# Performance work log

Hardware: AMD Instinct MI355X
Metric: run time of the kernel (lower is better)

The kernel has to match this reference:

```python
import jax, jax.numpy as jnp
from jax import lax
import numpy as np

T = 100  # number of binarization thresholds, as in nn.Module (linspace(0,1,100))
THRESHOLDS = jnp.linspace(0.0, 1.0, T)


def _count_components(binimg):
    """4-connected component count per image via iterative min-label propagation.
    binimg: [N,H,W] float in {0,1}. Returns [N] int32 component counts.
    Equivalent math to the source's recursive DFS flood fill, vectorized."""
    N, H, W = binimg.shape
    fg = binimg > 0
    BIG = H * W  # sentinel label for background
    idx = jnp.arange(H * W, dtype=jnp.int32).reshape(H, W)
    lab0 = jnp.where(fg, idx[None], jnp.int32(BIG))

    def prop(lab):
        p = jnp.pad(lab, ((0, 0), (1, 1), (1, 1)), constant_values=BIG)
        nmin = jnp.minimum(jnp.minimum(p[:, :-2, 1:-1], p[:, 2:, 1:-1]),
                           jnp.minimum(p[:, 1:-1, :-2], p[:, 1:-1, 2:]))
        return jnp.where(fg, jnp.minimum(lab, nmin), jnp.int32(BIG))

    def cond(c):
        return ~c[1]

    def body(c):
        lab = c[0]
        new = prop(prop(prop(lab)))  # 3 propagation steps per convergence check
        return (new, jnp.all(new == lab))

    lab, _ = lax.while_loop(cond, body, (lab0, jnp.array(False)))
    # each component keeps exactly one pixel whose label equals its own index
    return jnp.sum(fg & (lab == idx[None]), axis=(1, 2)).astype(jnp.int32)


def _betti(prob):
    """prob: [R,H,W] -> [T,R,2] (b0, b1) per threshold per region.
    b1 = b0 - euler, euler = #pixels - #4-neighbor edges (as in source)."""
    R, H, W = prob.shape
    binz = (prob[None] > THRESHOLDS[:, None, None, None]).astype(jnp.float32)  # [T,R,H,W]
    flat = binz.reshape(T * R, H, W)
    b0 = lax.stop_gradient(_count_components(flat)).astype(jnp.float32).reshape(T, R)
    pix = flat.sum((1, 2))
    edges = (flat[:, :-1] * flat[:, 1:]).sum((1, 2)) + (flat[:, :, :-1] * flat[:, :, 1:]).sum((1, 2))
    euler = (pix - edges).reshape(T, R)
    b1 = b0 - euler
    return jnp.stack([b0, b1], axis=-1)  # [T,R,2]


def setup_inputs() -> dict:
    key = jax.random.key(0)
    k1, k2 = jax.random.split(key)
    three_class_prob = jax.random.uniform(k1, (4, 3, 128, 128), dtype=jnp.float32)
    selected_regions = jnp.arange(4, dtype=jnp.int64)
    gt_barcodes = jax.random.uniform(k2, (4, 6, T - 1, 2), dtype=jnp.float32)
    return {"three_class_prob": three_class_prob,
            "selected_regions": selected_regions,
            "gt_barcodes": gt_barcodes}


def reference(three_class_prob, selected_regions, gt_barcodes):
    sel = three_class_prob[selected_regions]  # [R,3,H,W]
    inside = _betti(sel[:, 0])     # channel 0
    boundary = _betti(sel[:, 1])   # channel 1
    union = inside                 # source uses channel 0:1 again -> same values
    codes = jnp.concatenate([inside, boundary, union], axis=-1)  # [T,R,6]
    # barcode extraction: birth at increases of the betti curve, death at decreases
    d = codes[1:] - codes[:-1]                 # [T-1,R,6]
    th = THRESHOLDS[:-1, None, None]
    birth = jnp.where(d > 0, th, 0.0)
    death = jnp.where(d < 0, th, 0.0)
    barcodes = jnp.stack([birth, death], axis=-1).transpose(1, 2, 0, 3)  # [R,6,T-1,2]
    # fixed-shape matching: pair barcodes sorted by birth time (Hungarian surrogate)
    ord_b = jnp.argsort(barcodes[..., 0], axis=-1)
    ord_g = jnp.argsort(gt_barcodes[..., 0], axis=-1)
    bs = jnp.take_along_axis(barcodes, ord_b[..., None], axis=-2)
    gs = jnp.take_along_axis(gt_barcodes, ord_g[..., None], axis=-2)
    matched_diff = jnp.sum(jnp.abs(bs - gs), axis=-1)                  # [R,6,T-1]
    unmatched_len = jnp.sum(barcodes[..., 1] - barcodes[..., 0], axis=-1)  # [R,6]
    return jnp.mean(matched_diff) + jnp.mean(unmatched_len)
```

## Files before the change

### kernel.cpp

```cpp
#include <hip/hip_runtime.h>

typedef unsigned long long u64;

__device__ __forceinline__ int find_root(int* L, int a){
    int p = L[a];
    while(p != a){
        int gp = L[p];
        if(gp != p) L[a] = gp;
        a = p; p = gp;
    }
    return a;
}

__device__ __forceinline__ int unite(int* L, int a, int b){
    while(true){
        a = find_root(L, a);
        b = find_root(L, b);
        if(a == b) return 0;
        int hi = (a > b) ? a : b;
        int lo = (a > b) ? b : a;
        int old = atomicCAS(&L[hi], hi, lo);
        if(old == hi) return 1;
        a = old; b = lo;
    }
}

__global__ __launch_bounds__(256) void ccl_kernel(const float* __restrict__ prob,
                                                  const int*   __restrict__ sel,
                                                  float*       __restrict__ betti,
                                                  float*       __restrict__ out){
    __shared__ u64 M[256];
    __shared__ u64 S[256];
    __shared__ int Pr[257];
    __shared__ int L[6400];
    __shared__ int red[12];
    const int tid = threadIdx.x, bid = blockIdx.x;
    if(bid == 0 && tid == 0) atomicExch(out, 0.0f);
    const int ch = bid / 400, t = (bid % 400) >> 2, r = bid & 3;
    const float th = (float)t / 99.0f;
    const float* img = prob + (size_t)(sel[r] * 3 + ch) * 16384;

    const int w = tid;
    {
        const float4* imgv = (const float4*)img;
        u64 mw = 0ULL;
        #pragma unroll
        for(int k = 0; k < 16; k++){
            const float4 v = imgv[w * 16 + k];
            const unsigned nib = (unsigned)(v.x > th)
                               | ((unsigned)(v.y > th) << 1)
                               | ((unsigned)(v.z > th) << 2)
                               | ((unsigned)(v.w > th) << 3);
            mw |= (u64)nib << (4 * k);
        }
        M[w] = mw;
    }
    __syncthreads();

    const int lane = tid & 63, wave = tid >> 6;
    const int row = w >> 1, half = w & 1;
    const u64 m = M[w];
    const u64 lcar = half ? (M[w - 1] >> 63) : 0ULL;
    const u64 s = m & ~((m << 1) | lcar);
    S[w] = s;
    int pix   = __popcll(m);
    int edges = __popcll(m & ((m << 1) | lcar));
    const u64 va = (row > 0) ? M[w - 2] : 0ULL;
    edges += __popcll(m & va);
    const int runs = __popcll(s);
    u64 csm = 0ULL;
    if(row > 0){
        const u64 c = m & va;
        const u64 ccar = half ? ((M[w - 1] & M[w - 3]) >> 63) : 0ULL;
        csm = c & ~((c << 1) | ccar);
    }

    int incl = runs;
    for(int off = 1; off < 64; off <<= 1){
        int n = __shfl_up(incl, off, 64);
        if(lane >= off) incl += n;
    }
    if(lane == 63) red[wave] = incl;
    __syncthreads();
    int woff = 0;
    for(int k = 0; k < wave; k++) woff += red[k];
    const int excl = woff + incl - runs;
    Pr[w] = excl;
    if(w == 255) Pr[256] = excl + runs;
    const u64 sa = (row > 0) ? S[w - 2] : 0ULL;
    __syncthreads();
    const int R = Pr[256];
    const int Pa = (row > 0) ? Pr[w - 2] : 0;

    {
        int4* L4 = (int4*)L;
        const int n4 = (R + 3) >> 2;
        for(int i = tid; i < n4; i += 256){ int b = i * 4; L4[i] = make_int4(b, b+1, b+2, b+3); }
    }
    __syncthreads();

    int merges = 0;
    {
        u64 cs = csm;
        while(cs){
            const int x = __ffsll(cs) - 1;
            cs &= cs - 1;
            const u64 lm = (2ULL << x) - 1;
            const int nb = excl + __popcll(s  & lm) - 1;
            const int na = Pa   + __popcll(sa & lm) - 1;
            merges += unite(L, na, nb);
        }
    }

    int v0 = pix, v1 = edges, v2 = merges;
    for(int off = 32; off; off >>= 1){
        v0 += __shfl_down(v0, off, 64);
        v1 += __shfl_down(v1, off, 64);
        v2 += __shfl_down(v2, off, 64);
    }
    __syncthreads();
    if(lane == 0){ red[wave*3] = v0; red[wave*3+1] = v1; red[wave*3+2] = v2; }
    __syncthreads();
    if(tid == 0){
        int P = 0, E = 0, MG = 0;
        for(int k = 0; k < 4; k++){ P += red[k*3]; E += red[k*3+1]; MG += red[k*3+2]; }
        const float b0f = (float)(R - MG);
        const float b1f = b0f - ((float)P - (float)E);
        const size_t o = (((size_t)ch * 100 + t) * 4 + r) * 2;
        betti[o] = b0f; betti[o + 1] = b1f;
    }
}

__global__ __launch_bounds__(128) void rows_kernel(const float* __restrict__ betti,
                                                   const float* __restrict__ gt,
                                                   float*       __restrict__ out){
    __shared__ float codes[100];
    __shared__ float birth[99], bs0[99], bs1[99], gs0[99], gs1[99];
    __shared__ float gsh[198];
    __shared__ float red[4];
    const int row = blockIdx.x;
    const int r = row / 6, j = row % 6;
    const int chmap[6] = {0, 0, 1, 1, 0, 0};
    const int ch = chmap[j], comp = j & 1;
    const int tid = threadIdx.x;

    if(tid < 100) codes[tid] = betti[(((size_t)ch * 100 + tid) * 4 + r) * 2 + comp];
    const float* g = gt + (size_t)row * 99 * 2;
    for(int i = tid; i < 198; i += 128) gsh[i] = g[i];
    __syncthreads();

    float b = 0.f, d = 0.f;
    if(tid < 99){
        const float dv = codes[tid + 1] - codes[tid];
        const float thv = (float)tid / 99.0f;
        b = (dv > 0.f) ? thv : 0.f;
        d = (dv < 0.f) ? thv : 0.f;
        birth[tid] = b;
    }
    __syncthreads();

    if(tid < 99){
        int zb = 0, tz = 0;
        for(int k = 0; k < 99; k++){
            const int z = (birth[k] == 0.f) ? 1 : 0;
            tz += z;
            if(k < tid) zb += z;
        }
        const int pos = (b == 0.f) ? zb : (tz + tid - zb);
        bs0[pos] = b; bs1[pos] = d;

        const float gb = gsh[tid * 2];
        int rank = 0;
        for(int k = 0; k < 99; k++){
            const float o = gsh[k * 2];
            rank += (o < gb || (o == gb && k < tid)) ? 1 : 0;
        }
        gs0[rank] = gb; gs1[rank] = gsh[tid * 2 + 1];
    }
    __syncthreads();

    float mm = 0.f, u = 0.f;
    if(tid < 99){
        mm = fabsf(bs0[tid] - gs0[tid]) + fabsf(bs1[tid] - gs1[tid]);
        u = d - b;
    }
    for(int off = 32; off; off >>= 1){
        mm += __shfl_down(mm, off, 64);
        u  += __shfl_down(u,  off, 64);
    }
    if((tid & 63) == 0){ red[(tid >> 6)*2] = mm; red[(tid >> 6)*2 + 1] = u; }
    __syncthreads();
    if(tid == 0)
        atomicAdd(out, (red[0] + red[2]) / 2376.0f + (red[1] + red[3]) / 24.0f);
}

extern "C" void kernel_launch(void* const* d_in, const int* in_sizes, int n_in,
                              void* d_out, int out_size, void* d_ws, size_t ws_size,
                              hipStream_t stream){
    const float* prob = (const float*)d_in[0];
    const int*   sel  = (const int*)d_in[1];
    const float* gt   = (const float*)d_in[2];
    float* betti = (float*)d_ws;

    ccl_kernel <<<800, 256, 0, stream>>>(prob, sel, betti, (float*)d_out);
    rows_kernel<<<24, 128, 0, stream>>>(betti, gt, (float*)d_out);
}
```

Measured before the change: 92.82 us.

## Compact vertical merge edges into per-wave shared lists before union-find

Each thread used to walk its own vertical run-overlap bits and call union-find serially, so lanes with many overlaps held back their whole wave. The change packs each wave's edge count into the existing prefix scan, writes every merge pair into a per-wave shared buffer (capacity 512), and then spreads the unite calls evenly across the 64 lanes. Pairs beyond the capacity fall back to the old inline path. This adds shared memory, which can lower occupancy, plus an extra barrier.

New measurement: 97.01 us. 4.5% more time.

```diff
diff --git a/kernel.cpp b/kernel.cpp
--- a/kernel.cpp
+++ b/kernel.cpp
@@ -1,6 +1,8 @@
 #include <hip/hip_runtime.h>
 
 typedef unsigned long long u64;
+
+#define ECAP 512
 
 __device__ __forceinline__ int find_root(int* L, int a){
     int p = L[a];
@@ -33,6 +35,7 @@
     __shared__ u64 S[256];
     __shared__ int Pr[257];
     __shared__ int L[6400];
+    __shared__ unsigned E[4*ECAP];
     __shared__ int red[12];
     const int tid = threadIdx.x, bid = blockIdx.x;
     if(bid == 0 && tid == 0) atomicExch(out, 0.0f);
@@ -74,17 +77,20 @@
         const u64 ccar = half ? ((M[w - 1] & M[w - 3]) >> 63) : 0ULL;
         csm = c & ~((c << 1) | ccar);
     }
-
-    int incl = runs;
+    const int cw = __popcll(csm);
+
+    int incl = runs | (cw << 16);
     for(int off = 1; off < 64; off <<= 1){
         int n = __shfl_up(incl, off, 64);
         if(lane >= off) incl += n;
     }
-    if(lane == 63) red[wave] = incl;
+    if(lane == 63) red[wave] = incl & 0xFFFF;
+    const int ewt = (__shfl(incl, 63, 64)) >> 16;
     __syncthreads();
     int woff = 0;
     for(int k = 0; k < wave; k++) woff += red[k];
-    const int excl = woff + incl - runs;
+    const int excl  = woff + (incl & 0xFFFF) - runs;
+    const int ebase = (incl >> 16) - cw;
     Pr[w] = excl;
     if(w == 255) Pr[256] = excl + runs;
     const u64 sa = (row > 0) ? S[w - 2] : 0ULL;
@@ -102,13 +108,25 @@
     int merges = 0;
     {
         u64 cs = csm;
+        int bi = ebase;
         while(cs){
             const int x = __ffsll(cs) - 1;
             cs &= cs - 1;
             const u64 lm = (2ULL << x) - 1;
             const int nb = excl + __popcll(s  & lm) - 1;
             const int na = Pa   + __popcll(sa & lm) - 1;
-            merges += unite(L, na, nb);
+            if(bi < ECAP) E[wave * ECAP + bi] = ((unsigned)na << 13) | (unsigned)nb;
+            else merges += unite(L, na, nb);
+            bi++;
+        }
+    }
+    __syncthreads();
+
+    {
+        const int ew = ewt < ECAP ? ewt : ECAP;
+        for(int j = lane; j < ew; j += 64){
+            const unsigned e = E[wave * ECAP + j];
+            merges += unite(L, (int)(e >> 13), (int)(e & 8191u));
         }
     }
 
@@ -122,10 +140,10 @@
     if(lane == 0){ red[wave*3] = v0; red[wave*3+1] = v1; red[wave*3+2] = v2; }
     __syncthreads();
     if(tid == 0){
-        int P = 0, E = 0, MG = 0;
-        for(int k = 0; k < 4; k++){ P += red[k*3]; E += red[k*3+1]; MG += red[k*3+2]; }
+        int P = 0, Eh = 0, MG = 0;
+        for(int k = 0; k < 4; k++){ P += red[k*3]; Eh += red[k*3+1]; MG += red[k*3+2]; }
         const float b0f = (float)(R - MG);
-        const float b1f = b0f - ((float)P - (float)E);
+        const float b1f = b0f - ((float)P - (float)Eh);
         const size_t o = (((size_t)ch * 100 + t) * 4 + r) * 2;
         betti[o] = b0f; betti[o + 1] = b1f;
     }
```

## Split CCL into half-image blocks with a separate seam-merge kernel

Applied to the files above, without the earlier changes.

Each 128x128 binarized image is now labeled by two 128-thread blocks, one per half. The boundary-row root labels, masks and per-half statistics go to workspace, and a new merge kernel unites components across the seam to compute b0 and b1. This doubles block count and shrinks shared memory per block to raise occupancy and parallelism. It costs an extra kernel launch, global round trips for the labels, and serial bit-skipping loops in the merge.

New measurement: 97.28 us. 1.05x slower.

```diff
diff --git a/kernel.cpp b/kernel.cpp
--- a/kernel.cpp
+++ b/kernel.cpp
@@ -25,24 +25,27 @@
     }
 }
 
-__global__ __launch_bounds__(256) void ccl_kernel(const float* __restrict__ prob,
-                                                  const int*   __restrict__ sel,
-                                                  float*       __restrict__ betti,
-                                                  float*       __restrict__ out){
-    __shared__ u64 M[256];
-    __shared__ u64 S[256];
-    __shared__ int Pr[257];
-    __shared__ int L[6400];
-    __shared__ int red[12];
+__global__ __launch_bounds__(128) void ccl_half(const float* __restrict__ prob,
+                                                const int*   __restrict__ sel,
+                                                int*   __restrict__ labs,
+                                                u64*   __restrict__ bmask,
+                                                int*   __restrict__ stats,
+                                                float* __restrict__ out){
+    __shared__ u64 M[128];
+    __shared__ u64 S[128];
+    __shared__ int Pr[129];
+    __shared__ int L[4096];
+    __shared__ int red[8];
     const int tid = threadIdx.x, bid = blockIdx.x;
     if(bid == 0 && tid == 0) atomicExch(out, 0.0f);
-    const int ch = bid / 400, t = (bid % 400) >> 2, r = bid & 3;
+    const int ib = bid >> 1, h = bid & 1;
+    const int ch = ib / 400, t = (ib % 400) >> 2, r = ib & 3;
     const float th = (float)t / 99.0f;
     const float* img = prob + (size_t)(sel[r] * 3 + ch) * 16384;
+    const float4* imgv = (const float4*)img + h * 2048;
 
     const int w = tid;
     {
-        const float4* imgv = (const float4*)img;
         u64 mw = 0ULL;
         #pragma unroll
         for(int k = 0; k < 16; k++){
@@ -58,18 +61,18 @@
     __syncthreads();
 
     const int lane = tid & 63, wave = tid >> 6;
-    const int row = w >> 1, half = w & 1;
+    const int lrow = w >> 1, half = w & 1;
     const u64 m = M[w];
     const u64 lcar = half ? (M[w - 1] >> 63) : 0ULL;
     const u64 s = m & ~((m << 1) | lcar);
     S[w] = s;
     int pix   = __popcll(m);
     int edges = __popcll(m & ((m << 1) | lcar));
-    const u64 va = (row > 0) ? M[w - 2] : 0ULL;
+    const u64 va = (lrow > 0) ? M[w - 2] : 0ULL;
     edges += __popcll(m & va);
     const int runs = __popcll(s);
     u64 csm = 0ULL;
-    if(row > 0){
+    if(lrow > 0){
         const u64 c = m & va;
         const u64 ccar = half ? ((M[w - 1] & M[w - 3]) >> 63) : 0ULL;
         csm = c & ~((c << 1) | ccar);
@@ -82,20 +85,19 @@
     }
     if(lane == 63) red[wave] = incl;
     __syncthreads();
-    int woff = 0;
-    for(int k = 0; k < wave; k++) woff += red[k];
+    const int woff = wave ? red[0] : 0;
     const int excl = woff + incl - runs;
     Pr[w] = excl;
-    if(w == 255) Pr[256] = excl + runs;
-    const u64 sa = (row > 0) ? S[w - 2] : 0ULL;
-    __syncthreads();
-    const int R = Pr[256];
-    const int Pa = (row > 0) ? Pr[w - 2] : 0;
+    if(w == 127) Pr[128] = excl + runs;
+    const u64 sa = (lrow > 0) ? S[w - 2] : 0ULL;
+    __syncthreads();
+    const int R = Pr[128];
+    const int Pa = (lrow > 0) ? Pr[w - 2] : 0;
 
     {
         int4* L4 = (int4*)L;
         const int n4 = (R + 3) >> 2;
-        for(int i = tid; i < n4; i += 256){ int b = i * 4; L4[i] = make_int4(b, b+1, b+2, b+3); }
+        for(int i = tid; i < n4; i += 128){ int b = i * 4; L4[i] = make_int4(b, b+1, b+2, b+3); }
     }
     __syncthreads();
 
@@ -111,6 +113,18 @@
             merges += unite(L, na, nb);
         }
     }
+    __syncthreads();
+
+    {
+        const int lo    = h ? 0 : Pr[126];
+        const int hiEnd = h ? Pr[2] : R;
+        for(int i = lo + tid; i < hiEnd; i += 128)
+            labs[(size_t)bid * 64 + (i - lo)] = find_root(L, i);
+        if(tid < 2){
+            const int bw = h ? tid : (126 + tid);
+            bmask[(size_t)bid * 2 + tid] = M[bw];
+        }
+    }
 
     int v0 = pix, v1 = edges, v2 = merges;
     for(int off = 32; off; off >>= 1){
@@ -122,10 +136,61 @@
     if(lane == 0){ red[wave*3] = v0; red[wave*3+1] = v1; red[wave*3+2] = v2; }
     __syncthreads();
     if(tid == 0){
-        int P = 0, E = 0, MG = 0;
-        for(int k = 0; k < 4; k++){ P += red[k*3]; E += red[k*3+1]; MG += red[k*3+2]; }
-        const float b0f = (float)(R - MG);
-        const float b1f = b0f - ((float)P - (float)E);
+        stats[(size_t)bid*3 + 0] = red[0] + red[3];
+        stats[(size_t)bid*3 + 1] = red[1] + red[4];
+        stats[(size_t)bid*3 + 2] = R - (red[2] + red[5]);
+    }
+}
+
+__global__ __launch_bounds__(64) void merge_kernel(const int* __restrict__ labs,
+                                                   const u64* __restrict__ bmask,
+                                                   const int* __restrict__ stats,
+                                                   float*     __restrict__ betti){
+    __shared__ int A[8192];
+    __shared__ int TL[64], BL[64];
+    const int ib = blockIdx.x, tid = threadIdx.x;
+    const int tb = ib * 2, bb = ib * 2 + 1;
+    const u64 t0 = bmask[(size_t)tb*2], t1 = bmask[(size_t)tb*2+1];
+    const u64 b0m = bmask[(size_t)bb*2], b1m = bmask[(size_t)bb*2+1];
+    const u64 st0 = t0 & ~(t0 << 1);
+    const u64 st1 = t1 & ~((t1 << 1) | (t0 >> 63));
+    const u64 sb0 = b0m & ~(b0m << 1);
+    const u64 sb1 = b1m & ~((b1m << 1) | (b0m >> 63));
+    const int nT = __popcll(st0) + __popcll(st1);
+    const int nB = __popcll(sb0) + __popcll(sb1);
+    if(tid < nT) TL[tid] = labs[(size_t)tb*64 + tid];
+    if(tid < nB) BL[tid] = labs[(size_t)bb*64 + tid];
+    __syncthreads();
+    if(tid < nT){ const int l = TL[tid];        A[l] = l; }
+    if(tid < nB){ const int l = BL[tid] + 4096; A[l] = l; }
+    __syncthreads();
+
+    const u64 c0 = t0 & b0m, c1 = t1 & b1m;
+    const u64 cs0 = c0 & ~(c0 << 1);
+    const u64 cs1 = c1 & ~((c1 << 1) | (c0 >> 63));
+    const int n0 = __popcll(cs0), nC = n0 + __popcll(cs1);
+    const int seamE = __popcll(c0) + __popcll(c1);
+
+    int merges = 0;
+    for(int j = tid; j < nC; j += 64){
+        u64 cs; int k, wv;
+        if(j < n0){ cs = cs0; wv = 0; k = j; } else { cs = cs1; wv = 1; k = j - n0; }
+        for(int q = 0; q < k; q++) cs &= cs - 1;
+        const int x = __ffsll(cs) - 1;
+        const u64 lm = (2ULL << x) - 1;
+        int it, ibx;
+        if(wv == 0){ it = __popcll(st0 & lm) - 1;                 ibx = __popcll(sb0 & lm) - 1; }
+        else       { it = __popcll(st0) + __popcll(st1 & lm) - 1; ibx = __popcll(sb0) + __popcll(sb1 & lm) - 1; }
+        merges += unite(A, TL[it], BL[ibx] + 4096);
+    }
+    for(int off = 32; off; off >>= 1) merges += __shfl_down(merges, off, 64);
+    if(tid == 0){
+        const int pix   = stats[(size_t)tb*3]   + stats[(size_t)bb*3];
+        const int edges = stats[(size_t)tb*3+1] + stats[(size_t)bb*3+1] + seamE;
+        const int b0    = stats[(size_t)tb*3+2] + stats[(size_t)bb*3+2] - merges;
+        const int ch = ib / 400, t = (ib % 400) >> 2, r = ib & 3;
+        const float b0f = (float)b0;
+        const float b1f = b0f - ((float)pix - (float)edges);
         const size_t o = (((size_t)ch * 100 + t) * 4 + r) * 2;
         betti[o] = b0f; betti[o + 1] = b1f;
     }
@@ -201,7 +266,12 @@
     const int*   sel  = (const int*)d_in[1];
     const float* gt   = (const float*)d_in[2];
     float* betti = (float*)d_ws;
-
-    ccl_kernel <<<800, 256, 0, stream>>>(prob, sel, betti, (float*)d_out);
-    rows_kernel<<<24, 128, 0, stream>>>(betti, gt, (float*)d_out);
-}
+    int*   wsI   = (int*)d_ws;
+    int*   labs  = wsI + 2048;
+    u64*   bmask = (u64*)(wsI + 104448);
+    int*   stats = wsI + 110848;
+
+    ccl_half    <<<1600, 128, 0, stream>>>(prob, sel, labs, bmask, stats, (float*)d_out);
+    merge_kernel<<<800, 64, 0, stream>>>(labs, bmask, stats, betti);
+    rows_kernel <<<24, 128, 0, stream>>>(betti, gt, (float*)d_out);
+}
```
